# Optimization experiments

Hardware: AMD Instinct MI355X
Metric: run time of the kernel (lower is better)

## Reference

```python
import jax, jax.numpy as jnp
import numpy as np

N = 100_000          # number of nodes
E = 3_200_000        # number of edges (avg degree 32)
IN_CH = 128
OUT_CH = 128


def setup_inputs() -> dict:
    key = jax.random.key(0)
    k1, k2, k3, k4 = jax.random.split(key, 4)
    x = jax.random.normal(k1, (N, IN_CH), dtype=jnp.float32)
    edge_index = jax.random.randint(k2, (2, E), 0, N, dtype=jnp.int32)
    # torch nn.Linear weights have shape [out_features, in_features]
    W_theta = jax.random.normal(k3, (OUT_CH, IN_CH), dtype=jnp.float32) / np.sqrt(IN_CH).astype(np.float32)
    W_phi = jax.random.normal(k4, (OUT_CH, OUT_CH), dtype=jnp.float32) / np.sqrt(OUT_CH).astype(np.float32)
    return {"x": x, "edge_index": edge_index, "W_theta": W_theta, "W_phi": W_phi}


def reference(x, edge_index, W_theta, W_phi):
    row, col = edge_index[0], edge_index[1]
    rel_pos = x[row] - x[col]                       # [E, in]
    rel_t = rel_pos @ W_theta.T                     # [E, out]
    aggr = jax.ops.segment_max(rel_t, row, num_segments=N)  # [N, out], -inf for empty segments
    # torch_scatter.scatter_max leaves empty segments at 0
    aggr = jnp.where(jnp.isneginf(aggr), jnp.zeros((), dtype=aggr.dtype), aggr)
    return aggr @ W_phi.T                           # [N, out]
```

## Files before the change

### kernel.cpp

```cpp
#include <hip/hip_runtime.h>
#include <stdint.h>

#define N_NODES 100000
#define N_EDGES 3200000
#define CH 128
#define NBUK 391
#define CAP 8704
#define SPLIT_BLOCKS 391
#define ROWS_A 50048

typedef __bf16 bf16x8 __attribute__((ext_vector_type(8)));
typedef float  floatx4 __attribute__((ext_vector_type(4)));

__device__ __forceinline__ unsigned short f2bf_bits(float f) {
    unsigned u = __float_as_uint(f);
    u += 0x7FFFu + ((u >> 16) & 1u);
    return (unsigned short)(u >> 16);
}

__device__ __forceinline__ unsigned short enc16(unsigned short b) {
    return b ^ ((b & 0x8000u) ? 0xFFFFu : 0x8000u);
}

__device__ __forceinline__ unsigned pkminu(unsigned a, unsigned b) {
    unsigned d;
    asm("v_pk_min_u16 %0, %1, %2" : "=v"(d) : "v"(a), "v"(b));
    return d;
}

__device__ __forceinline__ unsigned dec2(unsigned k) {
    unsigned lo = k & 0xFFFFu;
    unsigned hi = k >> 16;
    lo ^= (lo & 0x8000u) ? 0x8000u : 0xFFFFu;
    hi ^= (hi & 0x8000u) ? 0x8000u : 0xFFFFu;
    return lo | (hi << 16);
}

__device__ __forceinline__ bf16x8 pack8(floatx4 f0, floatx4 f1) {
    bf16x8 r;
    r[0] = (__bf16)f0[0]; r[1] = (__bf16)f0[1]; r[2] = (__bf16)f0[2]; r[3] = (__bf16)f0[3];
    r[4] = (__bf16)f1[0]; r[5] = (__bf16)f1[1]; r[6] = (__bf16)f1[2]; r[7] = (__bf16)f1[3];
    return r;
}

__device__ __forceinline__ void gemm_tile(int row0, int lane, const float* __restrict__ x,
                                          const unsigned short* __restrict__ wb,
                                          unsigned short* __restrict__ yt) {
    int m = lane & 15, quad = lane >> 4;
    bf16x8 a[4];
    const floatx4* xp = (const floatx4*)(x + (size_t)(row0 + m) * CH + quad * 8);
#pragma unroll
    for (int ks = 0; ks < 4; ks++) a[ks] = pack8(xp[ks * 8], xp[ks * 8 + 1]);

    for (int nt = 0; nt < 8; nt++) {
        const bf16x8* wp = (const bf16x8*)(wb + (size_t)(nt * 16 + m) * CH + quad * 8);
        floatx4 acc = {0.f, 0.f, 0.f, 0.f};
#pragma unroll
        for (int ks = 0; ks < 4; ks++)
            acc = __builtin_amdgcn_mfma_f32_16x16x32_bf16(a[ks], wp[ks * 4], acc, 0, 0, 0);
#pragma unroll
        for (int r = 0; r < 4; r++) {
            int orow = row0 + quad * 4 + r;
            yt[(size_t)orow * CH + nt * 16 + m] = enc16(f2bf_bits(acc[r]));
        }
    }
}

__global__ void k_setup(const float* __restrict__ Wt, const float* __restrict__ Wp,
                        unsigned short* __restrict__ wb, int* __restrict__ cursor) {
    int bid = blockIdx.x, t = threadIdx.x;
    if (bid < 128) {
        int i = bid * 256 + t;
        float v = (i < 16384) ? Wt[i] : Wp[i - 16384];
        wb[i] = f2bf_bits(v);
    } else {
        for (int i = t; i < NBUK; i += 256) cursor[i] = i * CAP;
    }
}

__global__ void k_split_gemmyA(const int* __restrict__ row, const int* __restrict__ col,
                               int* __restrict__ cursor, unsigned* __restrict__ pairs,
                               const float* __restrict__ x,
                               const unsigned short* __restrict__ wb,
                               unsigned short* __restrict__ yt) {
    __shared__ int h[NBUK];
    __shared__ int basebuf[NBUK];
    int bid = blockIdx.x, t = threadIdx.x;
    if (bid < SPLIT_BLOCKS) {
        for (int i = t; i < NBUK; i += 256) h[i] = 0;
        __syncthreads();
        int e0 = bid * 8192;
        int4 r[8];
        bool v[8];
#pragma unroll
        for (int j = 0; j < 8; j++) {
            int idx = e0 + j * 1024 + t * 4;
            v[j] = idx < N_EDGES;
            if (v[j]) {
                r[j] = *(const int4*)(row + idx);
                atomicAdd(&h[r[j].x >> 8], 1);
                atomicAdd(&h[r[j].y >> 8], 1);
                atomicAdd(&h[r[j].z >> 8], 1);
                atomicAdd(&h[r[j].w >> 8], 1);
            }
        }
        __syncthreads();
        for (int i = t; i < NBUK; i += 256) {
            int c = h[i];
            basebuf[i] = c ? atomicAdd(&cursor[i], c) : 0;
            h[i] = 0;
        }
        __syncthreads();
#pragma unroll
        for (int j = 0; j < 8; j++) {
            if (v[j]) {
                int idx = e0 + j * 1024 + t * 4;
                int4 c = *(const int4*)(col + idx);
                int b, p;
                b = r[j].x >> 8; p = basebuf[b] + atomicAdd(&h[b], 1);
                if (p < (b + 1) * CAP) pairs[p] = ((unsigned)(r[j].x & 255) << 17) | (unsigned)c.x;
                b = r[j].y >> 8; p = basebuf[b] + atomicAdd(&h[b], 1);
                if (p < (b + 1) * CAP) pairs[p] = ((unsigned)(r[j].y & 255) << 17) | (unsigned)c.y;
                b = r[j].z >> 8; p = basebuf[b] + atomicAdd(&h[b], 1);
                if (p < (b + 1) * CAP) pairs[p] = ((unsigned)(r[j].z & 255) << 17) | (unsigned)c.z;
                b = r[j].w >> 8; p = basebuf[b] + atomicAdd(&h[b], 1);
                if (p < (b + 1) * CAP) pairs[p] = ((unsigned)(r[j].w & 255) << 17) | (unsigned)c.w;
            }
        }
    } else {
        int wave = (bid - SPLIT_BLOCKS) * 4 + (t >> 6);
        int row0 = wave * 16;
        if (row0 >= ROWS_A) return;
        gemm_tile(row0, t & 63, x, wb, yt);
    }
}

__global__ void k_build_gemmyB(unsigned* __restrict__ pairs, const int* __restrict__ cursor,
                               int* __restrict__ deg, int* __restrict__ offs,
                               const float* __restrict__ x,
                               const unsigned short* __restrict__ wb,
                               unsigned short* __restrict__ yt) {
    __shared__ int hist[256];
    __shared__ int sc[256];
    __shared__ int cur[256];
    __shared__ int lcsr[CAP];
    int bid = blockIdx.x, t = threadIdx.x;
    if (bid < NBUK) {
        int b = bid;
        int s0 = b * CAP;
        int cnt = cursor[b] - s0;
        if (cnt > CAP) cnt = CAP;
        if (t < 256) hist[t] = 0;
        __syncthreads();
        for (int i = t; i < cnt; i += 1024) {
            unsigned p = pairs[s0 + i];
            atomicAdd(&hist[p >> 17], 1);
        }
        __syncthreads();
        int d = 0;
        if (t < 256) { d = hist[t]; sc[t] = d; }
        __syncthreads();
        for (int off = 1; off < 256; off <<= 1) {
            int vv = 0;
            if (t < 256 && t >= off) vv = sc[t - off];
            __syncthreads();
            if (t < 256) sc[t] += vv;
            __syncthreads();
        }
        if (t < 256) {
            int excl = sc[t] - d;
            int node = b * 256 + t;
            if (node < N_NODES) {
                deg[node] = d;
                offs[node] = s0 + excl;
            }
            cur[t] = excl;
        }
        __syncthreads();
        for (int i = t; i < cnt; i += 1024) {
            unsigned p = pairs[s0 + i];
            int pos = atomicAdd(&cur[p >> 17], 1);
            lcsr[pos] = (int)(p & 0x1FFFFu);
        }
        __syncthreads();
        int* csr = (int*)pairs;
        for (int i = t; i < cnt; i += 1024) csr[s0 + i] = lcsr[i];
    } else {
        int wg = (bid - NBUK) * 16 + (t >> 6);
        int row0 = ROWS_A + wg * 16;
        if (row0 >= N_NODES) return;
        gemm_tile(row0, t & 63, x, wb, yt);
    }
}

#define PKA(v)                        \
    do {                              \
        m0 = pkminu(m0, (v).x);       \
        m1 = pkminu(m1, (v).y);       \
        m2 = pkminu(m2, (v).z);       \
        m3 = pkminu(m3, (v).w);       \
    } while (0)

__global__ void k_minaggr_out(const uint4* __restrict__ yt, const int* __restrict__ offs,
                              const int* __restrict__ deg, const int* __restrict__ csr,
                              const unsigned short* __restrict__ wb,
                              float* __restrict__ out) {
    __shared__ unsigned short atile[16 * 136];
    int t = threadIdx.x;
    int wave = t >> 6, lane = t & 63;
    int q = lane >> 4, s = lane & 15;
    int nl = wave * 4 + q;
    int n = blockIdx.x * 16 + nl;

    int i = offs[n];
    int len = deg[n];
    int end = i + len;

    unsigned m0 = ~0u, m1 = ~0u, m2 = ~0u, m3 = ~0u;

    for (; i + 8 <= end; i += 8) {
        int c0 = csr[i + 0];
        int c1 = csr[i + 1];
        int c2 = csr[i + 2];
        int c3 = csr[i + 3];
        int c4 = csr[i + 4];
        int c5 = csr[i + 5];
        int c6 = csr[i + 6];
        int c7 = csr[i + 7];
        uint4 v0 = yt[(size_t)c0 * 16 + s];
        uint4 v1 = yt[(size_t)c1 * 16 + s];
        uint4 v2 = yt[(size_t)c2 * 16 + s];
        uint4 v3 = yt[(size_t)c3 * 16 + s];
        uint4 v4 = yt[(size_t)c4 * 16 + s];
        uint4 v5 = yt[(size_t)c5 * 16 + s];
        uint4 v6 = yt[(size_t)c6 * 16 + s];
        uint4 v7 = yt[(size_t)c7 * 16 + s];
        PKA(v0); PKA(v1); PKA(v2); PKA(v3);
        PKA(v4); PKA(v5); PKA(v6); PKA(v7);
    }
    for (; i < end; i++) {
        int c = csr[i];
        uint4 v = yt[(size_t)c * 16 + s];
        PKA(v);
    }

    uint4 outv = {0u, 0u, 0u, 0u};
    if (len > 0) {
        unsigned d0 = dec2(m0), d1 = dec2(m1), d2 = dec2(m2), d3 = dec2(m3);
        uint4 se = yt[(size_t)n * 16 + s];
        unsigned s0 = dec2(se.x), s1 = dec2(se.y), s2 = dec2(se.z), s3 = dec2(se.w);
        outv.x = (unsigned)f2bf_bits(__uint_as_float(s0 << 16) - __uint_as_float(d0 << 16)) |
                 ((unsigned)f2bf_bits(__uint_as_float(s0 & 0xFFFF0000u) -
                                      __uint_as_float(d0 & 0xFFFF0000u)) << 16);
        outv.y = (unsigned)f2bf_bits(__uint_as_float(s1 << 16) - __uint_as_float(d1 << 16)) |
                 ((unsigned)f2bf_bits(__uint_as_float(s1 & 0xFFFF0000u) -
                                      __uint_as_float(d1 & 0xFFFF0000u)) << 16);
        outv.z = (unsigned)f2bf_bits(__uint_as_float(s2 << 16) - __uint_as_float(d2 << 16)) |
                 ((unsigned)f2bf_bits(__uint_as_float(s2 & 0xFFFF0000u) -
                                      __uint_as_float(d2 & 0xFFFF0000u)) << 16);
        outv.w = (unsigned)f2bf_bits(__uint_as_float(s3 << 16) - __uint_as_float(d3 << 16)) |
                 ((unsigned)f2bf_bits(__uint_as_float(s3 & 0xFFFF0000u) -
                                      __uint_as_float(d3 & 0xFFFF0000u)) << 16);
    }
    *(uint4*)&atile[nl * 136 + s * 8] = outv;
    __syncthreads();

    int m = lane & 15, quad = lane >> 4;
    bf16x8 a[4];
#pragma unroll
    for (int ks = 0; ks < 4; ks++)
        a[ks] = *(const bf16x8*)&atile[m * 136 + ks * 32 + quad * 8];

#pragma unroll
    for (int ntl = 0; ntl < 2; ntl++) {
        int nt = wave * 2 + ntl;
        const bf16x8* wp = (const bf16x8*)(wb + (size_t)(nt * 16 + m) * CH + quad * 8);
        floatx4 acc = {0.f, 0.f, 0.f, 0.f};
#pragma unroll
        for (int ks = 0; ks < 4; ks++)
            acc = __builtin_amdgcn_mfma_f32_16x16x32_bf16(a[ks], wp[ks * 4], acc, 0, 0, 0);
#pragma unroll
        for (int r = 0; r < 4; r++)
            out[(size_t)(blockIdx.x * 16 + quad * 4 + r) * CH + nt * 16 + m] = acc[r];
    }
}

extern "C" void kernel_launch(void* const* d_in, const int* in_sizes, int n_in,
                              void* d_out, int out_size, void* d_ws, size_t ws_size,
                              hipStream_t stream) {
    const float* x   = (const float*)d_in[0];
    const int* edge  = (const int*)d_in[1];
    const float* Wt  = (const float*)d_in[2];
    const float* Wp  = (const float*)d_in[3];
    const int* row = edge;
    const int* col = edge + N_EDGES;
    float* out = (float*)d_out;

    char* ws = (char*)d_ws;
    int* deg    = (int*)ws;  ws += 400128;
    int* offs   = (int*)ws;  ws += 400128;
    int* cursor = (int*)ws;  ws += 2048;
    unsigned short* yt = (unsigned short*)ws; ws += 25600000;
    unsigned short* wb = (unsigned short*)ws; ws += 65536;
    unsigned* pairs = (unsigned*)ws; ws += (size_t)NBUK * CAP * 4;

    k_setup<<<129, 256, 0, stream>>>(Wt, Wp, wb, cursor);
    k_split_gemmyA<<<SPLIT_BLOCKS + 782, 256, 0, stream>>>(row, col, cursor, pairs,
                                                           x, wb, yt);
    k_build_gemmyB<<<NBUK + 196, 1024, 0, stream>>>(pairs, cursor, deg, offs, x, wb, yt);
    k_minaggr_out<<<N_NODES / 16, 256, 0, stream>>>((const uint4*)yt, offs, deg,
                                                    (const int*)pairs, wb + 16384, out);
}
```

Before: 296.9 us.

## Stage bucketed edge pairs in shared memory before contiguous global writes

The split phase now uses twice as many blocks with half the edges each. Each block sorts its pairs locally into shared memory by bucket, using a prefix scan over the bucket histogram. It then copies each bucket's run to global memory as a contiguous segment, replacing scattered per-edge global writes. This should improve write coalescing, at the cost of extra shared memory, a 512-wide block scan, and serial per-bucket copy loops run by one thread each.

```diff
diff --git a/kernel.cpp b/kernel.cpp
--- a/kernel.cpp
+++ b/kernel.cpp
@@ -6,7 +6,8 @@
 #define CH 128
 #define NBUK 391
 #define CAP 8704
-#define SPLIT_BLOCKS 391
+#define SPLITB 782
+#define EPB 4096
 #define ROWS_A 50048
 
 typedef __bf16 bf16x8 __attribute__((ext_vector_type(8)));
@@ -83,17 +84,21 @@
                                const float* __restrict__ x,
                                const unsigned short* __restrict__ wb,
                                unsigned short* __restrict__ yt) {
+    __shared__ unsigned lpair[EPB];
     __shared__ int h[NBUK];
-    __shared__ int basebuf[NBUK];
+    __shared__ int hb[NBUK];
+    __shared__ int lbase[NBUK];
+    __shared__ int cur[NBUK];
+    __shared__ int sc[512];
     int bid = blockIdx.x, t = threadIdx.x;
-    if (bid < SPLIT_BLOCKS) {
+    if (bid < SPLITB) {
         for (int i = t; i < NBUK; i += 256) h[i] = 0;
         __syncthreads();
-        int e0 = bid * 8192;
-        int4 r[8];
-        bool v[8];
-#pragma unroll
-        for (int j = 0; j < 8; j++) {
+        int e0 = bid * EPB;
+        int4 r[4];
+        bool v[4];
+#pragma unroll
+        for (int j = 0; j < 4; j++) {
             int idx = e0 + j * 1024 + t * 4;
             v[j] = idx < N_EDGES;
             if (v[j]) {
@@ -107,28 +112,53 @@
         __syncthreads();
         for (int i = t; i < NBUK; i += 256) {
             int c = h[i];
-            basebuf[i] = c ? atomicAdd(&cursor[i], c) : 0;
-            h[i] = 0;
-        }
-        __syncthreads();
-#pragma unroll
-        for (int j = 0; j < 8; j++) {
+            hb[i] = c ? atomicAdd(&cursor[i], c) : 0;
+        }
+        sc[t] = h[t];
+        sc[t + 256] = (t + 256 < NBUK) ? h[t + 256] : 0;
+        __syncthreads();
+        for (int off = 1; off < 512; off <<= 1) {
+            int a0 = (t >= off) ? sc[t - off] : 0;
+            int a1 = (t + 256 >= off) ? sc[t + 256 - off] : 0;
+            __syncthreads();
+            sc[t] += a0;
+            sc[t + 256] += a1;
+            __syncthreads();
+        }
+        for (int i = t; i < NBUK; i += 256) {
+            int lb = sc[i] - h[i];
+            lbase[i] = lb;
+            cur[i] = lb;
+        }
+        __syncthreads();
+#pragma unroll
+        for (int j = 0; j < 4; j++) {
             if (v[j]) {
                 int idx = e0 + j * 1024 + t * 4;
                 int4 c = *(const int4*)(col + idx);
                 int b, p;
-                b = r[j].x >> 8; p = basebuf[b] + atomicAdd(&h[b], 1);
-                if (p < (b + 1) * CAP) pairs[p] = ((unsigned)(r[j].x & 255) << 17) | (unsigned)c.x;
-                b = r[j].y >> 8; p = basebuf[b] + atomicAdd(&h[b], 1);
-                if (p < (b + 1) * CAP) pairs[p] = ((unsigned)(r[j].y & 255) << 17) | (unsigned)c.y;
-                b = r[j].z >> 8; p = basebuf[b] + atomicAdd(&h[b], 1);
-                if (p < (b + 1) * CAP) pairs[p] = ((unsigned)(r[j].z & 255) << 17) | (unsigned)c.z;
-                b = r[j].w >> 8; p = basebuf[b] + atomicAdd(&h[b], 1);
-                if (p < (b + 1) * CAP) pairs[p] = ((unsigned)(r[j].w & 255) << 17) | (unsigned)c.w;
+                b = r[j].x >> 8; p = atomicAdd(&cur[b], 1);
+                lpair[p] = ((unsigned)(r[j].x & 255) << 17) | (unsigned)c.x;
+                b = r[j].y >> 8; p = atomicAdd(&cur[b], 1);
+                lpair[p] = ((unsigned)(r[j].y & 255) << 17) | (unsigned)c.y;
+                b = r[j].z >> 8; p = atomicAdd(&cur[b], 1);
+                lpair[p] = ((unsigned)(r[j].z & 255) << 17) | (unsigned)c.z;
+                b = r[j].w >> 8; p = atomicAdd(&cur[b], 1);
+                lpair[p] = ((unsigned)(r[j].w & 255) << 17) | (unsigned)c.w;
             }
         }
+        __syncthreads();
+        for (int b = t; b < NBUK; b += 256) {
+            int n = h[b];
+            if (!n) continue;
+            int src = lbase[b];
+            int dst = hb[b];
+            int lim = (b + 1) * CAP - dst;
+            if (n > lim) n = lim;
+            for (int k = 0; k < n; k++) pairs[dst + k] = lpair[src + k];
+        }
     } else {
-        int wave = (bid - SPLIT_BLOCKS) * 4 + (t >> 6);
+        int wave = (bid - SPLITB) * 4 + (t >> 6);
         int row0 = wave * 16;
         if (row0 >= ROWS_A) return;
         gemm_tile(row0, t & 63, x, wb, yt);
@@ -305,8 +335,8 @@
     unsigned* pairs = (unsigned*)ws; ws += (size_t)NBUK * CAP * 4;
 
     k_setup<<<129, 256, 0, stream>>>(Wt, Wp, wb, cursor);
-    k_split_gemmyA<<<SPLIT_BLOCKS + 782, 256, 0, stream>>>(row, col, cursor, pairs,
-                                                           x, wb, yt);
+    k_split_gemmyA<<<SPLITB + 782, 256, 0, stream>>>(row, col, cursor, pairs,
+                                                     x, wb, yt);
     k_build_gemmyB<<<NBUK + 196, 1024, 0, stream>>>(pairs, cursor, deg, offs, x, wb, yt);
     k_minaggr_out<<<N_NODES / 16, 256, 0, stream>>>((const uint4*)yt, offs, deg,
                                                     (const int*)pairs, wb + 16384, out);
```

Result: no change. 296.1 us (-0.3%).
